# Kernel tuning notes

Measured on AMD Instinct MI355X. Metric: run time of the kernel, lower is better.

Reference implementation:

```python
import jax, jax.numpy as jnp
import numpy as np

NUM_BINS = 36
MIN_ACTIVATION = 0.1
PENALTY_WEIGHT = 1.0


def setup_inputs() -> dict:
    key = jax.random.key(0)
    k1, k2 = jax.random.split(key)
    mask = jax.random.uniform(k1, (64, 1, 640, 640), dtype=jnp.float32)
    bbox = jax.random.uniform(k2, (64, 4), dtype=jnp.float32)
    return {"mask": mask, "bbox": bbox}


def reference(mask, bbox):
    B, _, H, W = mask.shape
    nb = NUM_BINS
    # pixel-space bbox centers
    cx = bbox[:, 0] * W  # (B,)
    cy = bbox[:, 1] * H  # (B,)
    x = jnp.arange(W, dtype=jnp.float32)
    y = jnp.arange(H, dtype=jnp.float32)
    # (B, H, W) offsets from each sample's center
    dx = x[None, None, :] - cx[:, None, None]
    dy = y[None, :, None] - cy[:, None, None]
    angles = jnp.arctan2(dy, dx)  # (B, H, W) in [-pi, pi]
    binf = (angles + jnp.pi) / (2.0 * jnp.pi) * nb
    bins = jnp.clip(binf.astype(jnp.int32), 0, nb - 1)  # (B, H, W)
    # fused per-(sample, bin) segment mean via a single scatter-add pass
    seg = (bins + jnp.arange(B, dtype=jnp.int32)[:, None, None] * nb).reshape(-1)
    m = mask[:, 0].reshape(-1)
    sums = jax.ops.segment_sum(m, seg, num_segments=B * nb)
    cnts = jax.ops.segment_sum(jnp.ones_like(m), seg, num_segments=B * nb)
    act = jnp.where(cnts > 0, sums / jnp.maximum(cnts, 1.0), 0.0).reshape(B, nb)
    under = (act < MIN_ACTIVATION).astype(jnp.float32)
    penalty_per_sample = under.sum(axis=1) / nb
    return PENALTY_WEIGHT * penalty_per_sample.mean()
```

## Files before the change

kernel.cpp:

```cpp
#include <hip/hip_runtime.h>
#include <math.h>

#define NB 36
#define W 640
#define H 640
#define NSAMP 64
#define RPB 40
#define BPS 16
#define NBLK (NSAMP * BPS)
#define PSTRIDE 40
#define FIX_SCALE 4194304.0f
#define INV_FIX (1.0f/4194304.0f)
#define CNT_SHIFT 44
#define SUM_MASK ((1ull << CNT_SHIFT) - 1)
#define AMB 1e-6

__device__ __constant__ double COT[36] = {
    0.0,
    5.6712818196177095,  2.7474774194546223,  1.7320508075688773,
    1.1917535925942100,  0.8390996311772800,  0.5773502691896258,
    0.3639702342662024,  0.1763269807084650,  0.0,
    -0.1763269807084650, -0.3639702342662024, -0.5773502691896258,
    -0.8390996311772800, -1.1917535925942100, -1.7320508075688773,
    -2.7474774194546223, -5.6712818196177095,
    0.0,
    5.6712818196177095,  2.7474774194546223,  1.7320508075688773,
    1.1917535925942100,  0.8390996311772800,  0.5773502691896258,
    0.3639702342662024,  0.1763269807084650,  0.0,
    -0.1763269807084650, -0.3639702342662024, -0.5773502691896258,
    -0.8390996311772800, -1.1917535925942100, -1.7320508075688773,
    -2.7474774194546223, -5.6712818196177095
};

__device__ __forceinline__ int bin_slow(int x, int y, double cxd, double cyd) {
    const double PI_D    = 3.141592653589793;
    const double TWOPI_D = 6.283185307179586;
    double t  = (atan2((double)y - cyd, (double)x - cxd) + PI_D) / TWOPI_D;
    double bd = t * 36.0;
    int k = (int)bd;
    k = k < 0 ? 0 : k;
    return k > NB - 1 ? NB - 1 : k;
}

#define SCAN_STEP(x, ctrl, rmask)                                             \
    x += (unsigned)__builtin_amdgcn_update_dpp(0, (int)(x), (ctrl), (rmask),  \
                                               0xf, false)

__global__ __launch_bounds__(256) void acl_main(const float* __restrict__ mask,
                                                const float* __restrict__ bbox,
                                                unsigned long long* __restrict__ ws) {
    __shared__ int A_l[RPB][18];
    __shared__ int sgn_l[RPB];
    __shared__ __align__(16) unsigned srow[4][768];
    __shared__ unsigned long long lbin[NB];

    const int tid = threadIdx.x;
    const int b   = blockIdx.x >> 4;
    const int rg  = blockIdx.x & (BPS - 1);
    const int y0  = rg * RPB;

    if (tid < NB) lbin[tid] = 0ull;
    if (tid < RPB) A_l[tid][17] = W - 1;

    const double cxd = (double)bbox[b * 4 + 0] * 640.0;
    const double cyd = (double)bbox[b * 4 + 1] * 640.0;

    for (int task = tid; task < RPB * 17; task += 256) {
        const int rl = task / 17, mi = task % 17;
        const int y  = y0 + rl;
        const double dy = (double)y - cyd;
        int i, a;
        if (dy == 0.0) {
            if (mi == 0) sgn_l[rl] = 0;
            i = mi;
            a = (mi == 0) ? ((int)ceil(cxd) - 1) : (W - 1);
        } else {
            const bool dp = (dy > 0.0);
            if (mi == 0) sgn_l[rl] = dp ? 1 : -1;
            const int m = dp ? (19 + mi) : (1 + mi);
            double x = cxd + dy * COT[m];
            x = fmin(fmax(x, -2.0), 642.0);
            double g  = x + 2.0;
            int    gi = (int)g;
            double fr = g - (double)gi;
            int v = dp ? (gi - 2)
                       : (gi - 1);
            if (fr < AMB || fr > 1.0 - AMB) {
                int xa = (int)(x + 2.5) - 2;
                if (xa >= 0 && xa <= W - 1) {
                    int kb = bin_slow(xa, y, cxd, cyd);
                    if (dp) v = (kb >= m) ? xa : xa - 1;
                    else    v = (kb >= m) ? xa : xa + 1;
                }
            }
            if (dp) { i = 16 - mi; a = v; }
            else    { i = mi;      a = v - 1; }
        }
        a = a < -1 ? -1 : (a > W - 1 ? W - 1 : a);
        A_l[rl][i] = a;
    }
    __syncthreads();

    const int wid = tid >> 6, lane = tid & 63;
    const float* rowbase = mask + (size_t)b * (W * H) + (size_t)y0 * W;

    unsigned long long accPs = 0ull, accNs = 0ull;
    unsigned accPc = 0u, accNc = 0u;

    const float4 z4 = make_float4(0.f, 0.f, 0.f, 0.f);
    const float4* rpA = (const float4*)(rowbase + (size_t)wid * W);
    float4 a0 = rpA[lane], a1 = rpA[lane + 64];
    float4 a2 = (lane < 32) ? rpA[lane + 128] : z4;
    const float4* rpB = (const float4*)(rowbase + (size_t)(wid + 4) * W);
    float4 b0 = rpB[lane], b1 = rpB[lane + 64];
    float4 b2 = (lane < 32) ? rpB[lane + 128] : z4;

    for (int j = 0; j < 10; j++) {
        const int rl = wid + 4 * j;
        float4 n0, n1, n2;
        if (j < 8) {
            const float4* np = (const float4*)(rowbase + (size_t)(rl + 8) * W);
            n0 = np[lane];
            n1 = np[lane + 64];
            n2 = (lane < 32) ? np[lane + 128] : z4;
        }

        unsigned carry = 0u;
        #pragma unroll
        for (int s = 0; s < 3; s++) {
            const float4 v = (s == 0) ? a0 : (s == 1) ? a1 : a2;
            const unsigned q0 = __float2uint_rn(v.x * FIX_SCALE);
            const unsigned q1 = __float2uint_rn(v.y * FIX_SCALE);
            const unsigned q2 = __float2uint_rn(v.z * FIX_SCALE);
            const unsigned q3 = __float2uint_rn(v.w * FIX_SCALE);
            const unsigned p0 = q0, p1 = p0 + q1, p2 = p1 + q2, p3 = p2 + q3;

            unsigned x = p3;
            SCAN_STEP(x, 0x111, 0xf);
            SCAN_STEP(x, 0x112, 0xf);
            SCAN_STEP(x, 0x114, 0xf);
            SCAN_STEP(x, 0x118, 0xf);
            SCAN_STEP(x, 0x142, 0xa);
            SCAN_STEP(x, 0x143, 0xc);
            const unsigned base = carry + (x - p3);
            uint4 wv;
            wv.x = base + p0; wv.y = base + p1; wv.z = base + p2; wv.w = base + p3;
            *((uint4*)&srow[wid][s * 256 + lane * 4]) = wv;
            carry += (unsigned)__builtin_amdgcn_readlane((int)x, 63);
        }

        if (lane < 18) {
            const int aR = A_l[rl][lane];
            const int aL = (lane == 0) ? -1 : A_l[rl][lane - 1];
            const int cnt = aR - aL;
            if (cnt > 0) {
                const unsigned sR = srow[wid][aR];
                const unsigned sL = (aL >= 0) ? srow[wid][aL] : 0u;
                const unsigned seg = sR - sL;
                const int sg = sgn_l[rl];
                if (sg > 0)      { accPc += (unsigned)cnt; accPs += seg; }
                else if (sg < 0) { accNc += (unsigned)cnt; accNs += seg; }
                else atomicAdd(&lbin[(lane == 0) ? 35 : 18],
                               ((unsigned long long)cnt << CNT_SHIFT)
                               + (unsigned long long)seg);
            }
        }
        a0 = b0; a1 = b1; a2 = b2;
        b0 = n0; b1 = n1; b2 = n2;
    }

    if (lane < 18) {
        if (accPc) atomicAdd(&lbin[35 - lane],
                             ((unsigned long long)accPc << CNT_SHIFT) + accPs);
        if (accNc) atomicAdd(&lbin[lane],
                             ((unsigned long long)accNc << CNT_SHIFT) + accNs);
    }
    __syncthreads();
    if (tid < NB)
        ws[(size_t)blockIdx.x * PSTRIDE + tid] = lbin[tid];
}

__global__ __launch_bounds__(256) void acl_final(const unsigned long long* __restrict__ ws,
                                                 float* __restrict__ out) {
    __shared__ unsigned nund[256];
    __shared__ float s[NSAMP];
    const int tid = threadIdx.x;
    const int b = tid >> 2, q = tid & 3;
    unsigned cu = 0;
    #pragma unroll
    for (int kk = 0; kk < 9; kk++) {
        const int k = q * 9 + kk;
        unsigned long long tot = 0ull;
        #pragma unroll
        for (int g = 0; g < BPS; g++)
            tot += ws[(size_t)(b * BPS + g) * PSTRIDE + k];
        const unsigned long long cnt = tot >> CNT_SHIFT;
        const float sum = (float)(tot & SUM_MASK) * INV_FIX;
        const float act = (cnt != 0ull) ? (sum / (float)cnt) : 0.0f;
        if (act < 0.1f) cu++;
    }
    nund[tid] = cu;
    __syncthreads();
    if (tid < NSAMP) {
        const unsigned n = nund[4 * tid] + nund[4 * tid + 1]
                         + nund[4 * tid + 2] + nund[4 * tid + 3];
        s[tid] = (float)n / 36.0f;
    }
    __syncthreads();
    if (tid == 0) {
        float acc = 0.0f;
        for (int i = 0; i < NSAMP; i++) acc += s[i];
        out[0] = acc / 64.0f;
    }
}

extern "C" void kernel_launch(void* const* d_in, const int* in_sizes, int n_in,
                              void* d_out, int out_size, void* d_ws, size_t ws_size,
                              hipStream_t stream) {
    const float* mask = (const float*)d_in[0];
    const float* bbox = (const float*)d_in[1];
    unsigned long long* ws = (unsigned long long*)d_ws;

    acl_main<<<dim3(NBLK), dim3(256), 0, stream>>>(mask, bbox, ws);
    acl_final<<<dim3(1), dim3(256), 0, stream>>>(ws, (float*)d_out);
}
```

Baseline: 38.64 us.

## Halve rows per block, double blocks, and transpose workspace for coalesced final reduction

Each sample now gets 32 blocks of 20 rows instead of 16 blocks of 40. The two-row-deep register prefetch becomes a single-row prefetch, and launch bounds request 8 blocks per CU. The aim is more parallelism and occupancy for the memory-bound main pass. The partial-bin workspace is stored bin-major so the final kernel's loads are coalesced, and that reduction uses two accumulators. In exchange the final kernel reduces twice as many partials, and each block has less prefetch depth to hide memory latency.

```diff
diff --git a/kernel.cpp b/kernel.cpp
--- a/kernel.cpp
+++ b/kernel.cpp
@@ -5,10 +5,9 @@
 #define W 640
 #define H 640
 #define NSAMP 64
-#define RPB 40
-#define BPS 16
+#define RPB 20
+#define BPS 32
 #define NBLK (NSAMP * BPS)
-#define PSTRIDE 40
 #define FIX_SCALE 4194304.0f
 #define INV_FIX (1.0f/4194304.0f)
 #define CNT_SHIFT 44
@@ -46,16 +45,16 @@
     x += (unsigned)__builtin_amdgcn_update_dpp(0, (int)(x), (ctrl), (rmask),  \
                                                0xf, false)
 
-__global__ __launch_bounds__(256) void acl_main(const float* __restrict__ mask,
-                                                const float* __restrict__ bbox,
-                                                unsigned long long* __restrict__ ws) {
+__global__ __launch_bounds__(256, 8) void acl_main(const float* __restrict__ mask,
+                                                   const float* __restrict__ bbox,
+                                                   unsigned long long* __restrict__ ws) {
     __shared__ int A_l[RPB][18];
     __shared__ int sgn_l[RPB];
     __shared__ __align__(16) unsigned srow[4][768];
     __shared__ unsigned long long lbin[NB];
 
     const int tid = threadIdx.x;
-    const int b   = blockIdx.x >> 4;
+    const int b   = blockIdx.x >> 5;
     const int rg  = blockIdx.x & (BPS - 1);
     const int y0  = rg * RPB;
 
@@ -108,18 +107,15 @@
     unsigned accPc = 0u, accNc = 0u;
 
     const float4 z4 = make_float4(0.f, 0.f, 0.f, 0.f);
-    const float4* rpA = (const float4*)(rowbase + (size_t)wid * W);
-    float4 a0 = rpA[lane], a1 = rpA[lane + 64];
-    float4 a2 = (lane < 32) ? rpA[lane + 128] : z4;
-    const float4* rpB = (const float4*)(rowbase + (size_t)(wid + 4) * W);
-    float4 b0 = rpB[lane], b1 = rpB[lane + 64];
-    float4 b2 = (lane < 32) ? rpB[lane + 128] : z4;
-
-    for (int j = 0; j < 10; j++) {
+    const float4* rp0 = (const float4*)(rowbase + (size_t)wid * W);
+    float4 a0 = rp0[lane], a1 = rp0[lane + 64];
+    float4 a2 = (lane < 32) ? rp0[lane + 128] : z4;
+
+    for (int j = 0; j < 5; j++) {
         const int rl = wid + 4 * j;
         float4 n0, n1, n2;
-        if (j < 8) {
-            const float4* np = (const float4*)(rowbase + (size_t)(rl + 8) * W);
+        if (j < 4) {
+            const float4* np = (const float4*)(rowbase + (size_t)(rl + 4) * W);
             n0 = np[lane];
             n1 = np[lane + 64];
             n2 = (lane < 32) ? np[lane + 128] : z4;
@@ -165,8 +161,7 @@
                                + (unsigned long long)seg);
             }
         }
-        a0 = b0; a1 = b1; a2 = b2;
-        b0 = n0; b1 = n1; b2 = n2;
+        if (j < 4) { a0 = n0; a1 = n1; a2 = n2; }
     }
 
     if (lane < 18) {
@@ -177,7 +172,7 @@
     }
     __syncthreads();
     if (tid < NB)
-        ws[(size_t)blockIdx.x * PSTRIDE + tid] = lbin[tid];
+        ws[(size_t)tid * NBLK + blockIdx.x] = lbin[tid];
 }
 
 __global__ __launch_bounds__(256) void acl_final(const unsigned long long* __restrict__ ws,
@@ -185,15 +180,19 @@
     __shared__ unsigned nund[256];
     __shared__ float s[NSAMP];
     const int tid = threadIdx.x;
-    const int b = tid >> 2, q = tid & 3;
+    const int b = tid & 63, q = tid >> 6;
     unsigned cu = 0;
     #pragma unroll
     for (int kk = 0; kk < 9; kk++) {
         const int k = q * 9 + kk;
-        unsigned long long tot = 0ull;
+        const unsigned long long* base = ws + (size_t)k * NBLK + (size_t)b * BPS;
+        unsigned long long t0 = 0ull, t1 = 0ull;
         #pragma unroll
-        for (int g = 0; g < BPS; g++)
-            tot += ws[(size_t)(b * BPS + g) * PSTRIDE + k];
+        for (int g = 0; g < BPS; g += 2) {
+            t0 += base[g];
+            t1 += base[g + 1];
+        }
+        const unsigned long long tot = t0 + t1;
         const unsigned long long cnt = tot >> CNT_SHIFT;
         const float sum = (float)(tot & SUM_MASK) * INV_FIX;
         const float act = (cnt != 0ull) ? (sum / (float)cnt) : 0.0f;
@@ -202,8 +201,7 @@
     nund[tid] = cu;
     __syncthreads();
     if (tid < NSAMP) {
-        const unsigned n = nund[4 * tid] + nund[4 * tid + 1]
-                         + nund[4 * tid + 2] + nund[4 * tid + 3];
+        const unsigned n = nund[tid] + nund[64 + tid] + nund[128 + tid] + nund[192 + tid];
         s[tid] = (float)n / 36.0f;
     }
     __syncthreads();
```

After: 46.30 us. 1.2x slower.
